# Optimization experiments

Hardware: AMD Instinct MI355X
Metric: run time of the kernel (lower is better)

The kernel has to match this reference:

```python
import jax, jax.numpy as jnp
import numpy as np

DIM = 1024
NUM_HEADS = 16
HEAD_DIM = DIM // NUM_HEADS


def setup_inputs() -> dict:
    key = jax.random.key(0)
    k1, k2, k3, k4, k5, k6 = jax.random.split(key, 6)
    B, T, C = 4, 2048, DIM
    s = 1.0 / np.sqrt(C)
    return {
        "x": jax.random.normal(k1, (B, T, C), dtype=jnp.float32),
        "attn_bias": jax.random.normal(k2, (B, T, T), dtype=jnp.float32),
        "qkv_w": jax.random.uniform(k3, (3 * C, C), dtype=jnp.float32, minval=-s, maxval=s),
        "qkv_b": jax.random.uniform(k4, (3 * C,), dtype=jnp.float32, minval=-s, maxval=s),
        "out_w": jax.random.uniform(k5, (C, C), dtype=jnp.float32, minval=-s, maxval=s),
        "out_b": jax.random.uniform(k6, (C,), dtype=jnp.float32, minval=-s, maxval=s),
    }


def reference(x, attn_bias, qkv_w, qkv_b, out_w, out_b):
    B, T, C = x.shape
    H, D = NUM_HEADS, HEAD_DIM
    # fused QKV projection (torch Linear: x @ W^T + b)
    qkv = jnp.einsum('btc,fc->btf', x, qkv_w) + qkv_b  # [B,T,3C]
    q, k, v = jnp.split(qkv, 3, axis=-1)
    q = q.reshape(B, T, H, D).transpose(0, 2, 1, 3)  # [B,H,T,D]
    k = k.reshape(B, T, H, D).transpose(0, 2, 1, 3)
    v = v.reshape(B, T, H, D).transpose(0, 2, 1, 3)
    scores = jnp.einsum('bhtd,bhsd->bhts', q, k) / jnp.sqrt(jnp.float32(D))
    scores = scores + attn_bias[:, None, :, :]  # 3-D bias -> broadcast over heads
    attn = jax.nn.softmax(scores, axis=-1)
    out = jnp.einsum('bhts,bhsd->bhtd', attn, v)  # [B,H,T,D]
    out = out.transpose(0, 2, 1, 3).reshape(B, T, C)
    return jnp.einsum('btc,fc->btf', out, out_w) + out_b
```

## Files before the change

### kernel.cpp

```cpp
#include <hip/hip_runtime.h>

#define BATCH 4
#define SEQ   2048
#define CDIM  1024
#define HEADS 16
#define HDIM  64
#define N3    3072
#define NTOK  8192
#define QKP   2048
#define LOG2E 1.44269504f
#define QSC   0.18033688f

typedef __attribute__((ext_vector_type(4))) float    float4v;
typedef __attribute__((ext_vector_type(8))) short    short8;
typedef __attribute__((ext_vector_type(8))) __bf16   bf16x8;
typedef __attribute__((ext_vector_type(4))) _Float16 half4v;
typedef __attribute__((ext_vector_type(2))) _Float16 half2v;

__device__ __forceinline__ unsigned short f2bf(float f) {
    union { float f; unsigned int u; } x; x.f = f;
    unsigned int r = x.u + 0x7fffu + ((x.u >> 16) & 1u);
    return (unsigned short)(r >> 16);
}

__device__ __forceinline__ bf16x8 ld_bf8(const unsigned short* p) {
    short8 s = *(const short8*)p;
    return __builtin_bit_cast(bf16x8, s);
}

__device__ __forceinline__ void glds16(const void* g, void* l) {
    __builtin_amdgcn_global_load_lds(
        (const __attribute__((address_space(1))) void*)g,
        (__attribute__((address_space(3))) void*)l, 16, 0, 0);
}

__global__ void cast_f32_bf16(const float* __restrict__ in,
                              unsigned short* __restrict__ out, int n4) {
    int i = blockIdx.x * blockDim.x + threadIdx.x;
    if (i >= n4) return;
    float4v v = ((const float4v*)in)[i];
    ushort4 r;
    r.x = f2bf(v[0]); r.y = f2bf(v[1]); r.z = f2bf(v[2]); r.w = f2bf(v[3]);
    ((ushort4*)out)[i] = r;
}

__global__ __launch_bounds__(256, 3)
void gemm_bt(const unsigned short* __restrict__ A,
             const unsigned short* __restrict__ Bm,
             const float* __restrict__ bias,
             void* __restrict__ Cout,
             void* __restrict__ Cout2,
             int M, int N, int K, int mode)
{
    __shared__ alignas(16) unsigned short As[128 * 64];
    __shared__ alignas(16) unsigned short Bs[128 * 64];

    const int tid  = threadIdx.x;
    const int lane = tid & 63;
    const int wave = tid >> 6;
    const int wr = wave >> 1, wc = wave & 1;
    const int lm = lane & 15, quad = lane >> 4;
    const size_t m0 = (size_t)blockIdx.y * 128;
    const size_t n0 = (size_t)blockIdx.x * 128;

    const unsigned short* ag[4];
    const unsigned short* bg[4];
    unsigned short* la[4];
    unsigned short* lb[4];
#pragma unroll
    for (int i = 0; i < 4; i++) {
        int idx = tid + i * 256;
        int row = idx >> 3;
        int lc  = (idx & 7) ^ (row & 7);
        ag[i] = &A [(m0 + row) * K + lc * 8];
        bg[i] = &Bm[(n0 + row) * K + lc * 8];
        la[i] = &As[(idx & ~63) * 8];
        lb[i] = &Bs[(idx & ~63) * 8];
    }

    float4v acc[4][4];
#pragma unroll
    for (int i = 0; i < 4; i++)
#pragma unroll
        for (int j = 0; j < 4; j++) acc[i][j] = (float4v){0.f, 0.f, 0.f, 0.f};

    for (int k0 = 0; k0 < K; k0 += 64) {
#pragma unroll
        for (int i = 0; i < 4; i++) glds16(ag[i], la[i]);
#pragma unroll
        for (int i = 0; i < 4; i++) glds16(bg[i], lb[i]);
#pragma unroll
        for (int i = 0; i < 4; i++) { ag[i] += 64; bg[i] += 64; }
        __syncthreads();
#pragma unroll
        for (int kk = 0; kk < 2; kk++) {
            bf16x8 af[4], bfr[4];
#pragma unroll
            for (int t = 0; t < 4; t++) {
                int slot = ((quad + kk * 4) ^ (lm & 7)) * 8;
                af [t] = ld_bf8(&As[(wr * 64 + t * 16 + lm) * 64 + slot]);
                bfr[t] = ld_bf8(&Bs[(wc * 64 + t * 16 + lm) * 64 + slot]);
            }
#pragma unroll
            for (int ti = 0; ti < 4; ti++)
#pragma unroll
                for (int tj = 0; tj < 4; tj++)
                    acc[ti][tj] = __builtin_amdgcn_mfma_f32_16x16x32_bf16(
                        af[ti], bfr[tj], acc[ti][tj], 0, 0, 0);
        }
        __syncthreads();
    }

#pragma unroll
    for (int ti = 0; ti < 4; ti++) {
        size_t row = m0 + wr * 64 + ti * 16 + quad * 4;
#pragma unroll
        for (int tj = 0; tj < 4; tj++) {
            int col = (int)n0 + wc * 64 + tj * 16 + lm;
            float bv = bias[col];
            if (mode == 0) {
#pragma unroll
                for (int r = 0; r < 4; r++)
                    ((float*)Cout)[(row + r) * N + col] = acc[ti][tj][r] + bv;
            } else if (col < 2 * CDIM) {
                float scl = (col < CDIM) ? QSC : 1.0f;
#pragma unroll
                for (int r = 0; r < 4; r++)
                    ((unsigned short*)Cout)[(row + r) * QKP + col] =
                        f2bf((acc[ti][tj][r] + bv) * scl);
            } else {
                int hd = col - 2 * CDIM;
                int bb = (int)(row >> 11);
                int s  = (int)(row & 2047);
                half4v hv;
#pragma unroll
                for (int r = 0; r < 4; r++) hv[r] = (_Float16)(acc[ti][tj][r] + bv);
                *(half4v*)((unsigned short*)Cout2 +
                           ((size_t)bb * CDIM + hd) * SEQ + s) = hv;
            }
        }
    }
}

__global__ __launch_bounds__(256, 4)
void attn_kernel(const unsigned short* __restrict__ qk,
                 const unsigned short* __restrict__ vT,
                 const float* __restrict__ bias,
                 unsigned short* __restrict__ outp)
{
    __shared__ alignas(16) char smem[32768];
    float*          BiasS = (float*)smem;
    unsigned short* Qs    = (unsigned short*)smem;
    unsigned short* Ks    = (unsigned short*)(smem + 16384);
    unsigned short* Vts   = (unsigned short*)(smem + 24576);

    const int tid  = threadIdx.x;
    const int lane = tid & 63, wave = tid >> 6;
    const int lm = lane & 15, quad = lane >> 4;
    const int q0 = blockIdx.x * 64;
    const int bh = blockIdx.y;
    const int bb = bh >> 4, h = bh & 15;
    const size_t rowbase = (size_t)bb * SEQ;
    const unsigned short* vTh = vT + (size_t)bh * HDIM * SEQ;
    const float* biasb = bias + (size_t)bb * SEQ * SEQ + (size_t)q0 * SEQ;

#pragma unroll
    for (int i = 0; i < 2; i++) {
        int idx = tid + i * 256;
        int row = idx >> 3;
        int lc  = (idx & 7) ^ (row & 7);
        glds16(&qk[(rowbase + q0 + row) * QKP + h * 64 + lc * 8], &Qs[(idx & ~63) * 8]);
    }
    __syncthreads();
    bf16x8 bq[2];
#pragma unroll
    for (int kk = 0; kk < 2; kk++)
        bq[kk] = ld_bf8(&Qs[(wave * 16 + lm) * 64 + (((quad + kk * 4) ^ (lm & 7)) * 8)]);

    const unsigned short *kg0, *kg1, *vg0, *vg1;
    unsigned short *lk0, *lk1, *lv0, *lv1;
    {
        int idx = tid, row = idx >> 3, lc = (idx & 7) ^ (row & 7);
        kg0 = &qk[(rowbase + row) * QKP + CDIM + h * 64 + lc * 8];
        vg0 = &vTh[(size_t)row * SEQ + lc * 8];
        lk0 = &Ks[(idx & ~63) * 8];
        lv0 = &Vts[(idx & ~63) * 8];
        idx = tid + 256; row = idx >> 3; lc = (idx & 7) ^ (row & 7);
        kg1 = &qk[(rowbase + row) * QKP + CDIM + h * 64 + lc * 8];
        vg1 = &vTh[(size_t)row * SEQ + lc * 8];
        lk1 = &Ks[(idx & ~63) * 8];
        lv1 = &Vts[(idx & ~63) * 8];
    }
    const float* bgp[4];
    float*       lbp[4];
#pragma unroll
    for (int i = 0; i < 4; i++) {
        int idx = tid + i * 256;
        int row = idx >> 4;
        int lc  = (idx & 15) ^ (row & 15);
        bgp[i] = &biasb[(size_t)row * SEQ + lc * 4];
        lbp[i] = &BiasS[(idx & ~63) * 4];
    }

    const half4v vones = {(_Float16)1.f, (_Float16)1.f, (_Float16)1.f, (_Float16)1.f};
    float4v rs4 = (float4v){0.f, 0.f, 0.f, 0.f};
    float4v o[4];
#pragma unroll
    for (int t = 0; t < 4; t++) o[t] = (float4v){0.f, 0.f, 0.f, 0.f};

    for (int it = 0; it < SEQ / 64; ++it) {
        __syncthreads();
        glds16(kg0, lk0); glds16(kg1, lk1);
        glds16(vg0, lv0); glds16(vg1, lv1);
#pragma unroll
        for (int i = 0; i < 4; i++) glds16(bgp[i], lbp[i]);
        kg0 += 64 * QKP; kg1 += 64 * QKP;
        vg0 += 64; vg1 += 64;
#pragma unroll
        for (int i = 0; i < 4; i++) bgp[i] += 64;
        __syncthreads();

        float4v st[4];
#pragma unroll
        for (int tj = 0; tj < 4; tj++) {
            float4v bv = *(const float4v*)&BiasS[(wave * 16 + lm) * 64 +
                                                 (((tj * 4 + quad) ^ lm) * 4)];
            st[tj] = bv * LOG2E;
            bf16x8 ak0 = ld_bf8(&Ks[(tj * 16 + lm) * 64 + (((quad    ) ^ (lm & 7)) * 8)]);
            bf16x8 ak1 = ld_bf8(&Ks[(tj * 16 + lm) * 64 + (((quad + 4) ^ (lm & 7)) * 8)]);
            st[tj] = __builtin_amdgcn_mfma_f32_16x16x32_bf16(ak0, bq[0], st[tj], 0, 0, 0);
            st[tj] = __builtin_amdgcn_mfma_f32_16x16x32_bf16(ak1, bq[1], st[tj], 0, 0, 0);
        }

        half4v pa[4];
#pragma unroll
        for (int tj = 0; tj < 4; tj++) {
            float p0 = __builtin_amdgcn_exp2f(st[tj][0]);
            float p1 = __builtin_amdgcn_exp2f(st[tj][1]);
            float p2 = __builtin_amdgcn_exp2f(st[tj][2]);
            float p3 = __builtin_amdgcn_exp2f(st[tj][3]);
            half2v plo = __builtin_bit_cast(half2v, __builtin_amdgcn_cvt_pkrtz(p0, p1));
            half2v phi = __builtin_bit_cast(half2v, __builtin_amdgcn_cvt_pkrtz(p2, p3));
            pa[tj][0] = plo[0]; pa[tj][1] = plo[1];
            pa[tj][2] = phi[0]; pa[tj][3] = phi[1];
        }

#pragma unroll
        for (int tj = 0; tj < 4; tj++)
            rs4 = __builtin_amdgcn_mfma_f32_16x16x16f16(pa[tj], vones, rs4, 0, 0, 0);

#pragma unroll
        for (int tj = 0; tj < 4; tj++) {
            int c = tj * 4 + quad;
#pragma unroll
            for (int dt = 0; dt < 4; dt++) {
                int row = dt * 16 + lm;
                int off = (((c >> 1) ^ (lm & 7)) * 8) + (c & 1) * 4;
                half4v vb = *(const half4v*)&Vts[row * 64 + off];
                o[dt] = __builtin_amdgcn_mfma_f32_16x16x16f16(pa[tj], vb, o[dt], 0, 0, 0);
            }
        }
    }

    float i4[4];
#pragma unroll
    for (int r = 0; r < 4; r++) i4[r] = 1.0f / rs4[r];
#pragma unroll
    for (int dt = 0; dt < 4; dt++) {
        int col = h * 64 + dt * 16 + lm;
#pragma unroll
        for (int r = 0; r < 4; r++) {
            size_t trow = rowbase + q0 + wave * 16 + quad * 4 + r;
            outp[trow * CDIM + col] = f2bf(o[dt][r] * i4[r]);
        }
    }
}

extern "C" void kernel_launch(void* const* d_in, const int* in_sizes, int n_in,
                              void* d_out, int out_size, void* d_ws, size_t ws_size,
                              hipStream_t stream)
{
    const float* x         = (const float*)d_in[0];
    const float* attn_bias = (const float*)d_in[1];
    const float* qkv_w     = (const float*)d_in[2];
    const float* qkv_b     = (const float*)d_in[3];
    const float* out_w     = (const float*)d_in[4];
    const float* out_b     = (const float*)d_in[5];
    float* out = (float*)d_out;

    char* p = (char*)d_ws;
    unsigned short* x_bf   = (unsigned short*)p; p += (size_t)NTOK * CDIM * 2;
    unsigned short* wq_bf  = (unsigned short*)p; p += (size_t)N3 * CDIM * 2;
    unsigned short* wo_bf  = (unsigned short*)p; p += (size_t)CDIM * CDIM * 2;
    unsigned short* qk_bf  = (unsigned short*)p; p += (size_t)NTOK * QKP * 2;
    unsigned short* vT_f16 = (unsigned short*)p; p += (size_t)BATCH * CDIM * SEQ * 2;
    unsigned short* at_bf  = (unsigned short*)p;

    int n4;
    n4 = NTOK * CDIM / 4;
    cast_f32_bf16<<<(n4 + 255) / 256, 256, 0, stream>>>(x, x_bf, n4);
    n4 = N3 * CDIM / 4;
    cast_f32_bf16<<<(n4 + 255) / 256, 256, 0, stream>>>(qkv_w, wq_bf, n4);
    n4 = CDIM * CDIM / 4;
    cast_f32_bf16<<<(n4 + 255) / 256, 256, 0, stream>>>(out_w, wo_bf, n4);

    gemm_bt<<<dim3(N3 / 128, NTOK / 128), 256, 0, stream>>>(
        x_bf, wq_bf, qkv_b, qk_bf, vT_f16, NTOK, N3, CDIM, 1);

    attn_kernel<<<dim3(SEQ / 64, BATCH * HEADS), 256, 0, stream>>>(
        qk_bf, vT_f16, attn_bias, at_bf);

    gemm_bt<<<dim3(CDIM / 128, NTOK / 128), 256, 0, stream>>>(
        at_bf, wo_bf, out_b, out, nullptr, NTOK, CDIM, CDIM, 0);
}
```

Baseline: 353.2 us.

## Stage transposed V stores through LDS, swizzle GEMM block order, raise PV MFMA priority

The QKV GEMM's V-output epilogue now writes its half-precision tile into shared memory in two passes and reads it back transposed, so global stores become contiguous 16-byte rows along the sequence instead of scattered 8-byte writes. The GEMM also remaps workgroup indices with a stride-8 interleave, which changes which output tiles run concurrently and may improve L2 reuse or XCD locality. The attention kernel wraps the PV MFMA loop in s_setprio to favour matrix work while other waves load. Costs are extra barriers and LDS traffic in the epilogue, and the remap assumes the grid size is divisible by 8.

```diff
diff --git a/kernel.cpp b/kernel.cpp
--- a/kernel.cpp
+++ b/kernel.cpp
@@ -52,16 +52,24 @@
              void* __restrict__ Cout2,
              int M, int N, int K, int mode)
 {
-    __shared__ alignas(16) unsigned short As[128 * 64];
-    __shared__ alignas(16) unsigned short Bs[128 * 64];
+    __shared__ alignas(16) unsigned short SMEM[2 * 128 * 64];
+    unsigned short* As = SMEM;
+    unsigned short* Bs = SMEM + 128 * 64;
 
     const int tid  = threadIdx.x;
     const int lane = tid & 63;
     const int wave = tid >> 6;
     const int wr = wave >> 1, wc = wave & 1;
     const int lm = lane & 15, quad = lane >> 4;
-    const size_t m0 = (size_t)blockIdx.y * 128;
-    const size_t n0 = (size_t)blockIdx.x * 128;
+
+    const int nwg  = gridDim.x * gridDim.y;
+    const int d    = blockIdx.y * gridDim.x + blockIdx.x;
+    const int orig = (d & 7) * (nwg >> 3) + (d >> 3);
+    const int bix  = orig % gridDim.x;
+    const int biy  = orig / gridDim.x;
+
+    const size_t m0 = (size_t)biy * 128;
+    const size_t n0 = (size_t)bix * 128;
 
     const unsigned short* ag[4];
     const unsigned short* bg[4];
@@ -111,32 +119,71 @@
         __syncthreads();
     }
 
-#pragma unroll
-    for (int ti = 0; ti < 4; ti++) {
-        size_t row = m0 + wr * 64 + ti * 16 + quad * 4;
-#pragma unroll
-        for (int tj = 0; tj < 4; tj++) {
-            int col = (int)n0 + wc * 64 + tj * 16 + lm;
-            float bv = bias[col];
-            if (mode == 0) {
+    const bool vpath = (mode == 1) && ((int)n0 >= 2 * CDIM);
+
+    if (!vpath) {
+#pragma unroll
+        for (int ti = 0; ti < 4; ti++) {
+            size_t row = m0 + wr * 64 + ti * 16 + quad * 4;
+#pragma unroll
+            for (int tj = 0; tj < 4; tj++) {
+                int col = (int)n0 + wc * 64 + tj * 16 + lm;
+                float bv = bias[col];
+                if (mode == 0) {
+#pragma unroll
+                    for (int r = 0; r < 4; r++)
+                        ((float*)Cout)[(row + r) * N + col] = acc[ti][tj][r] + bv;
+                } else {
+                    float scl = (col < CDIM) ? QSC : 1.0f;
+#pragma unroll
+                    for (int r = 0; r < 4; r++)
+                        ((unsigned short*)Cout)[(row + r) * QKP + col] =
+                            f2bf((acc[ti][tj][r] + bv) * scl);
+                }
+            }
+        }
+    } else {
+        half4v hv[4][4];
+#pragma unroll
+        for (int ti = 0; ti < 4; ti++)
+#pragma unroll
+            for (int tj = 0; tj < 4; tj++) {
+                int col = (int)n0 + wc * 64 + tj * 16 + lm;
+                float bv = bias[col];
 #pragma unroll
                 for (int r = 0; r < 4; r++)
-                    ((float*)Cout)[(row + r) * N + col] = acc[ti][tj][r] + bv;
-            } else if (col < 2 * CDIM) {
-                float scl = (col < CDIM) ? QSC : 1.0f;
-#pragma unroll
-                for (int r = 0; r < 4; r++)
-                    ((unsigned short*)Cout)[(row + r) * QKP + col] =
-                        f2bf((acc[ti][tj][r] + bv) * scl);
-            } else {
-                int hd = col - 2 * CDIM;
-                int bb = (int)(row >> 11);
-                int s  = (int)(row & 2047);
-                half4v hv;
-#pragma unroll
-                for (int r = 0; r < 4; r++) hv[r] = (_Float16)(acc[ti][tj][r] + bv);
-                *(half4v*)((unsigned short*)Cout2 +
-                           ((size_t)bb * CDIM + hd) * SEQ + s) = hv;
+                    hv[ti][tj][r] = (_Float16)(acc[ti][tj][r] + bv);
+            }
+
+        const int bbv = (int)(m0 >> 11);
+        const int s0  = (int)(m0 & 2047);
+        unsigned short* LT = SMEM;
+
+#pragma unroll
+        for (int p = 0; p < 2; ++p) {
+            __syncthreads();
+            if (wc == p) {
+#pragma unroll
+                for (int ti = 0; ti < 4; ti++) {
+                    int ssb = wr * 64 + ti * 16 + quad * 4;
+                    int p16 = (ssb >> 3);
+                    int w8  = (ssb >> 2) & 1;
+#pragma unroll
+                    for (int tj = 0; tj < 4; tj++) {
+                        int dd = tj * 16 + lm;
+                        *(half4v*)&LT[dd * 136 + ((p16 ^ (dd & 15)) * 8) + w8 * 4] =
+                            hv[ti][tj];
+                    }
+                }
+            }
+            __syncthreads();
+#pragma unroll
+            for (int i = 0; i < 4; ++i) {
+                int dd   = i * 16 + (tid >> 4);
+                int ss16 = tid & 15;
+                short8 val = *(const short8*)&LT[dd * 136 + ((ss16 ^ (dd & 15)) * 8)];
+                size_t gr = (size_t)bbv * CDIM + ((int)n0 - 2 * CDIM) + p * 64 + dd;
+                *(short8*)((unsigned short*)Cout2 + gr * SEQ + s0 + ss16 * 8) = val;
             }
         }
     }
@@ -222,7 +269,7 @@
 
         float4v st[4];
 #pragma unroll
-        for (int tj = 0; tj < 4; tj++) {
+        for (int tj = 0; tj < 4; ++tj) {
             float4v bv = *(const float4v*)&BiasS[(wave * 16 + lm) * 64 +
                                                  (((tj * 4 + quad) ^ lm) * 4)];
             st[tj] = bv * LOG2E;
@@ -234,7 +281,7 @@
 
         half4v pa[4];
 #pragma unroll
-        for (int tj = 0; tj < 4; tj++) {
+        for (int tj = 0; tj < 4; ++tj) {
             float p0 = __builtin_amdgcn_exp2f(st[tj][0]);
             float p1 = __builtin_amdgcn_exp2f(st[tj][1]);
             float p2 = __builtin_amdgcn_exp2f(st[tj][2]);
@@ -246,20 +293,22 @@
         }
 
 #pragma unroll
-        for (int tj = 0; tj < 4; tj++)
+        for (int tj = 0; tj < 4; ++tj)
             rs4 = __builtin_amdgcn_mfma_f32_16x16x16f16(pa[tj], vones, rs4, 0, 0, 0);
 
-#pragma unroll
-        for (int tj = 0; tj < 4; tj++) {
+        __builtin_amdgcn_s_setprio(1);
+#pragma unroll
+        for (int tj = 0; tj < 4; ++tj) {
             int c = tj * 4 + quad;
 #pragma unroll
-            for (int dt = 0; dt < 4; dt++) {
+            for (int dt = 0; dt < 4; ++dt) {
                 int row = dt * 16 + lm;
                 int off = (((c >> 1) ^ (lm & 7)) * 8) + (c & 1) * 4;
                 half4v vb = *(const half4v*)&Vts[row * 64 + off];
                 o[dt] = __builtin_amdgcn_mfma_f32_16x16x16f16(pa[tj], vb, o[dt], 0, 0, 0);
             }
         }
+        __builtin_amdgcn_s_setprio(0);
     }
 
     float i4[4];
```

Measured after the change: 352.7 us. No clear change (-0.1%).
